# Optimization experiments

Hardware: AMD Instinct MI355X
Metric: run time of the kernel (lower is better)

The kernel has to match this reference:

```python
import jax, jax.numpy as jnp
import numpy as np

H, KV, D, HID = 8, 4, 256, 2560  # heads, kv heads, head_dim, hidden_size
S, L = 32, 8192                  # new seq_len, cache_len
EPS = 1e-6


def setup_inputs() -> dict:
    key = jax.random.key(0)
    ks = jax.random.split(key, 10)
    return {
        "hidden_states": jax.random.normal(ks[0], (S, HID), jnp.float32),
        "cos": jax.random.uniform(ks[1], (S, D), jnp.float32, -1.0, 1.0),
        "sin": jax.random.uniform(ks[2], (S, D), jnp.float32, -1.0, 1.0),
        "cache_k": jax.random.normal(ks[3], (KV, L, D), jnp.float32),
        "cache_v": jax.random.normal(ks[4], (KV, L, D), jnp.float32),
        "mask": jnp.zeros((1, S, L), jnp.float32),
        "W_q": jax.random.normal(ks[5], (HID, H * D), jnp.float32) * 0.02,
        "W_k": jax.random.normal(ks[6], (HID, KV * D), jnp.float32) * 0.02,
        "W_v": jax.random.normal(ks[7], (HID, KV * D), jnp.float32) * 0.02,
        "W_o": jax.random.normal(ks[8], (H * D, HID), jnp.float32) * 0.02,
        "q_norm_w": jnp.ones((D,), jnp.float32),
        "k_norm_w": jnp.ones((D,), jnp.float32),
        "v_norm_w": jnp.ones((D,), jnp.float32),
    }


def _rms(x, w):
    return x * jax.lax.rsqrt(jnp.mean(x * x, axis=-1, keepdims=True) + EPS) * w


def _rope(x, cos, sin):
    # x: [h, S, D]; cos/sin: [S, D] broadcast over head axis
    half = x.shape[-1] // 2
    rot = jnp.concatenate([-x[..., half:], x[..., :half]], axis=-1)
    return x * cos + rot * sin


def reference(hidden_states, cos, sin, cache_k, cache_v, mask,
              W_q, W_k, W_v, W_o, q_norm_w, k_norm_w, v_norm_w):
    G = H // KV  # kv groups
    s = hidden_states.shape[0]
    l = cache_k.shape[1]

    q = (hidden_states @ W_q).reshape(s, H, D).transpose(1, 0, 2)   # [H,S,D]
    q = _rope(_rms(q, q_norm_w), cos, sin)
    k = (hidden_states @ W_k).reshape(s, KV, D).transpose(1, 0, 2)  # [KV,S,D]
    k = _rope(_rms(k, k_norm_w), cos, sin)
    v = _rms((hidden_states @ W_v).reshape(s, KV, D).transpose(1, 0, 2), v_norm_w)

    # sliding-window KV cache roll: drop oldest s, append new
    ck = jnp.concatenate([cache_k[:, s:, :], k], axis=1)  # [KV,L,D]
    cv = jnp.concatenate([cache_v[:, s:, :], v], axis=1)  # [KV,L,D]

    qg = q.reshape(KV, G * s, D)
    attn = jnp.einsum('knd,kld->knl', qg, ck).reshape(H, s, l)  # no 1/sqrt(D), per source
    attn = jax.nn.softmax(attn + mask, axis=-1).reshape(KV, G * s, l)
    out = jnp.einsum('knl,kld->knd', attn, cv)                   # [KV,G*S,D]
    out = out.reshape(H, s, D).transpose(1, 0, 2).reshape(s, H * D)
    return out @ W_o
```

## Files before the change

kernel.cpp:

```cpp
#include <hip/hip_runtime.h>
#include <hip/hip_bf16.h>
#include <cstdint>
#include <cstddef>

#define H_     8
#define KV_    4
#define D_     256
#define HID_   2560
#define S_     32
#define L_     8192
#define NQ_    64
#define LKEEP_ (L_ - S_)

__global__ __launch_bounds__(256) void k_qkv(
    const float* __restrict__ hidden,
    const float* __restrict__ Wq, const float* __restrict__ Wk, const float* __restrict__ Wv,
    float* __restrict__ part)
{
    const int col0  = blockIdx.x * 512;
    const int kbase = blockIdx.y * 80;
    const float* W; int ldw, wb;
    if (col0 < 2048)      { W = Wq; ldw = 2048; wb = col0; }
    else if (col0 < 3072) { W = Wk; ldw = 1024; wb = col0 - 2048; }
    else                  { W = Wv; ldw = 1024; wb = col0 - 3072; }
    const int tid = threadIdx.x;
    const int tc  = tid * 2;

    __shared__ __align__(16) float hsT[80][36];
    for (int i = 0; i < 3; i++) {
        int idx = i * 256 + tid;
        if (idx < 640) {
            int r = idx / 20, c4 = idx % 20;
            float4 v = *(const float4*)&hidden[r * HID_ + kbase + c4 * 4];
            hsT[c4*4+0][r] = v.x; hsT[c4*4+1][r] = v.y;
            hsT[c4*4+2][r] = v.z; hsT[c4*4+3][r] = v.w;
        }
    }
    __syncthreads();

    const float* Wt = W + (size_t)kbase * ldw + wb + tc;
    float acc[32][2] = {};
#define LW(k) (*(const float2*)&Wt[(size_t)(k) * ldw])
#define FMABLK(k, wc) \
    _Pragma("unroll") for (int r4 = 0; r4 < 8; r4++) { \
      float4 h = *(const float4*)&hsT[(k)][r4*4]; \
      acc[r4*4+0][0] = fmaf(h.x, wc.x, acc[r4*4+0][0]); acc[r4*4+0][1] = fmaf(h.x, wc.y, acc[r4*4+0][1]); \
      acc[r4*4+1][0] = fmaf(h.y, wc.x, acc[r4*4+1][0]); acc[r4*4+1][1] = fmaf(h.y, wc.y, acc[r4*4+1][1]); \
      acc[r4*4+2][0] = fmaf(h.z, wc.x, acc[r4*4+2][0]); acc[r4*4+2][1] = fmaf(h.z, wc.y, acc[r4*4+2][1]); \
      acc[r4*4+3][0] = fmaf(h.w, wc.x, acc[r4*4+3][0]); acc[r4*4+3][1] = fmaf(h.w, wc.y, acc[r4*4+3][1]); }
#define STEPL(wreg, k) { float2 wc = wreg; wreg = LW((k) + 8); FMABLK(k, wc) }
#define STEPN(wreg, k) { float2 wc = wreg; FMABLK(k, wc) }

    float2 w0=LW(0),w1=LW(1),w2=LW(2),w3=LW(3),w4=LW(4),w5=LW(5),w6=LW(6),w7=LW(7);
    for (int ib = 0; ib <= 64; ib += 8) {
        STEPL(w0, ib+0) STEPL(w1, ib+1) STEPL(w2, ib+2) STEPL(w3, ib+3)
        STEPL(w4, ib+4) STEPL(w5, ib+5) STEPL(w6, ib+6) STEPL(w7, ib+7)
    }
    STEPN(w0, 72) STEPN(w1, 73) STEPN(w2, 74) STEPN(w3, 75)
    STEPN(w4, 76) STEPN(w5, 77) STEPN(w6, 78) STEPN(w7, 79)
#undef STEPL
#undef STEPN
#undef FMABLK
#undef LW
    float* op = part + (size_t)blockIdx.y * (32 * 4096);
    #pragma unroll
    for (int r = 0; r < 32; r++)
        *(float2*)&op[r * 4096 + col0 + tc] = make_float2(acc[r][0], acc[r][1]);
}

__global__ __launch_bounds__(256) void k_rms_rope(
    const float* __restrict__ part,
    const float* __restrict__ cosb, const float* __restrict__ sinb,
    const float* __restrict__ qw, const float* __restrict__ kw, const float* __restrict__ vw,
    float* __restrict__ q, float* __restrict__ kn, float* __restrict__ vn)
{
    const int b = blockIdx.x;
    const int th = b >> 5;
    const int s  = b & 31;
    const int d  = threadIdx.x;
    const float* w; float* op; int col; bool rope;
    if (th < 8)       { w = qw; col = th * 256;               op = q  + ((size_t)(th * 32 + s)) * 256;        rope = true;  }
    else if (th < 12) { w = kw; col = 2048 + (th - 8) * 256;  op = kn + ((size_t)((th - 8) * 32 + s)) * 256;  rope = true;  }
    else              { w = vw; col = 3072 + (th - 12) * 256; op = vn + ((size_t)((th - 12) * 32 + s)) * 256; rope = false; }
    const int base = s * 4096 + col + d;
    float a0 = 0.f, a1 = 0.f, a2 = 0.f, a3 = 0.f;
    #pragma unroll
    for (int p = 0; p < 32; p += 4) {
        a0 += part[(size_t)(p + 0) * 131072 + base];
        a1 += part[(size_t)(p + 1) * 131072 + base];
        a2 += part[(size_t)(p + 2) * 131072 + base];
        a3 += part[(size_t)(p + 3) * 131072 + base];
    }
    float x = (a0 + a1) + (a2 + a3);
    float ss = x * x;
    #pragma unroll
    for (int m = 32; m; m >>= 1) ss += __shfl_xor(ss, m, 64);
    __shared__ float red[4];
    __shared__ float xs[256];
    if ((threadIdx.x & 63) == 0) red[threadIdx.x >> 6] = ss;
    __syncthreads();
    float tot = red[0] + red[1] + red[2] + red[3];
    float xn = x * rsqrtf(tot * (1.0f / 256.0f) + 1e-6f) * w[d];
    xs[d] = xn;
    __syncthreads();
    float out = xn;
    if (rope) {
        float rot = (d < 128) ? -xs[d + 128] : xs[d - 128];
        out = xn * cosb[s * 256 + d] + rot * sinb[s * 256 + d];
    }
    op[d] = out;
}

__global__ __launch_bounds__(512) void k_qk(
    const float* __restrict__ qb,
    const float* __restrict__ cache_k,
    const float* __restrict__ knb,
    const float* __restrict__ mask,
    float* __restrict__ logits)
{
    const int l0 = blockIdx.x * 128;
    const int kh = blockIdx.y;
    const int tid = threadIdx.x;
    const int r0 = (tid >> 6) * 8;
    const int c0 = (tid & 63) * 2;

    __shared__ __align__(16) float ks[2][32][132];
    __shared__ __align__(16) float qsq[2][64][36];

    float acc[8][2] = {};

    {
        int qq = tid >> 3, dq = tid & 7;
        *(float4*)&qsq[0][qq][dq * 4] =
            *(const float4*)&qb[((size_t)kh * 64 + qq) * 256 + dq * 4];
        #pragma unroll
        for (int i = 0; i < 2; i++) {
            int idx = i * 512 + tid;
            int l = idx >> 3, d4 = idx & 7;
            int labs = l0 + l;
            const float* src = (labs < LKEEP_)
                ? (cache_k + ((size_t)kh * L_ + labs + S_) * 256 + d4 * 4)
                : (knb + ((size_t)kh * S_ + (labs - LKEEP_)) * 256 + d4 * 4);
            float4 v = *(const float4*)src;
            ks[0][d4 * 4 + 0][l] = v.x; ks[0][d4 * 4 + 1][l] = v.y;
            ks[0][d4 * 4 + 2][l] = v.z; ks[0][d4 * 4 + 3][l] = v.w;
        }
    }
    __syncthreads();

    for (int dc = 0; dc < 8; dc++) {
        const int cur = dc & 1, nxt = cur ^ 1;
        if (dc < 7) {
            const int d0 = (dc + 1) * 32;
            {
                int qq = tid >> 3, dq = tid & 7;
                *(float4*)&qsq[nxt][qq][dq * 4] =
                    *(const float4*)&qb[((size_t)kh * 64 + qq) * 256 + d0 + dq * 4];
            }
            #pragma unroll
            for (int i = 0; i < 2; i++) {
                int idx = i * 512 + tid;
                int l = idx >> 3, d4 = idx & 7;
                int labs = l0 + l;
                const float* src = (labs < LKEEP_)
                    ? (cache_k + ((size_t)kh * L_ + labs + S_) * 256 + d0 + d4 * 4)
                    : (knb + ((size_t)kh * S_ + (labs - LKEEP_)) * 256 + d0 + d4 * 4);
                float4 v = *(const float4*)src;
                ks[nxt][d4 * 4 + 0][l] = v.x; ks[nxt][d4 * 4 + 1][l] = v.y;
                ks[nxt][d4 * 4 + 2][l] = v.z; ks[nxt][d4 * 4 + 3][l] = v.w;
            }
        }
        #pragma unroll
        for (int d4 = 0; d4 < 8; d4++) {
            float4 qv[8];
            #pragma unroll
            for (int i = 0; i < 8; i++)
                qv[i] = *(const float4*)&qsq[cur][r0 + i][d4 * 4];
            float2 k0 = *(const float2*)&ks[cur][d4 * 4 + 0][c0];
            float2 k1 = *(const float2*)&ks[cur][d4 * 4 + 1][c0];
            float2 k2 = *(const float2*)&ks[cur][d4 * 4 + 2][c0];
            float2 k3 = *(const float2*)&ks[cur][d4 * 4 + 3][c0];
            #pragma unroll
            for (int i = 0; i < 8; i++) {
                acc[i][0] = fmaf(qv[i].x, k0.x, acc[i][0]); acc[i][1] = fmaf(qv[i].x, k0.y, acc[i][1]);
                acc[i][0] = fmaf(qv[i].y, k1.x, acc[i][0]); acc[i][1] = fmaf(qv[i].y, k1.y, acc[i][1]);
                acc[i][0] = fmaf(qv[i].z, k2.x, acc[i][0]); acc[i][1] = fmaf(qv[i].z, k2.y, acc[i][1]);
                acc[i][0] = fmaf(qv[i].w, k3.x, acc[i][0]); acc[i][1] = fmaf(qv[i].w, k3.y, acc[i][1]);
            }
        }
        __syncthreads();
    }
    #pragma unroll
    for (int i = 0; i < 8; i++) {
        int qq = r0 + i, s = qq & 31;
        float2 m2 = *(const float2*)&mask[(size_t)s * L_ + l0 + c0];
        *(float2*)&logits[((size_t)kh * NQ_ + qq) * L_ + l0 + c0] =
            make_float2(acc[i][0] + m2.x, acc[i][1] + m2.y);
    }
}

__global__ __launch_bounds__(256) void k_rowstat(
    const float* __restrict__ logits,
    float* __restrict__ rowmax, float* __restrict__ rowsum)
{
    const int r = blockIdx.x;
    const int tid = threadIdx.x;
    const float* lp = logits + (size_t)r * L_;
    float m = -1e30f, s = 0.f;
    for (int i = tid; i < L_; i += 256) {
        float x = lp[i];
        float nm = fmaxf(m, x);
        s = s * __expf(m - nm) + __expf(x - nm);
        m = nm;
    }
    #pragma unroll
    for (int off = 32; off; off >>= 1) {
        float m2 = __shfl_xor(m, off, 64);
        float s2 = __shfl_xor(s, off, 64);
        float nm = fmaxf(m, m2);
        s = s * __expf(m - nm) + s2 * __expf(m2 - nm);
        m = nm;
    }
    __shared__ float rm[4], rs[4];
    if ((tid & 63) == 0) { rm[tid >> 6] = m; rs[tid >> 6] = s; }
    __syncthreads();
    if (tid == 0) {
        float M = fmaxf(fmaxf(rm[0], rm[1]), fmaxf(rm[2], rm[3]));
        float S = rs[0] * __expf(rm[0] - M) + rs[1] * __expf(rm[1] - M)
                + rs[2] * __expf(rm[2] - M) + rs[3] * __expf(rm[3] - M);
        rowmax[r] = M;
        rowsum[r] = S;
    }
}

__global__ __launch_bounds__(512) void k_pv(
    const float* __restrict__ logits,
    const float* __restrict__ rowmax,
    const float* __restrict__ cache_v, const float* __restrict__ vnb,
    float* __restrict__ pvpart)
{
    const int l0 = blockIdx.x * 128;
    const int kh = blockIdx.y;
    const int tid = threadIdx.x;
    const int r0 = (tid >> 6) * 8;
    const int c0 = (tid & 63) * 4;

    __shared__ __align__(16) float ps[64][132];
    __shared__ __align__(16) float vs[2][16][260];

    #pragma unroll
    for (int i = 0; i < 4; i++) {
        int idx = i * 512 + tid;
        int qq = idx >> 5, lq = idx & 31;
        float4 v = *(const float4*)&logits[((size_t)kh * NQ_ + qq) * L_ + l0 + lq * 4];
        float rm = rowmax[kh * NQ_ + qq];
        v.x = __expf(v.x - rm); v.y = __expf(v.y - rm);
        v.z = __expf(v.z - rm); v.w = __expf(v.w - rm);
        *(float4*)&ps[qq][lq * 4] = v;
    }
    #pragma unroll
    for (int i = 0; i < 2; i++) {
        int idx = i * 512 + tid;
        int l = idx >> 6, dq = idx & 63;
        int labs = l0 + l;
        const float* src = (labs < LKEEP_)
            ? (cache_v + ((size_t)kh * L_ + labs + S_) * 256 + dq * 4)
            : (vnb + ((size_t)kh * S_ + (labs - LKEEP_)) * 256 + dq * 4);
        *(float4*)&vs[0][l][dq * 4] = *(const float4*)src;
    }
    __syncthreads();

    float acc[8][4] = {};
    for (int lc = 0; lc < 8; lc++) {
        const int cur = lc & 1, nxt = cur ^ 1;
        if (lc < 7) {
            #pragma unroll
            for (int i = 0; i < 2; i++) {
                int idx = i * 512 + tid;
                int l = idx >> 6, dq = idx & 63;
                int labs = l0 + (lc + 1) * 16 + l;
                const float* src = (labs < LKEEP_)
                    ? (cache_v + ((size_t)kh * L_ + labs + S_) * 256 + dq * 4)
                    : (vnb + ((size_t)kh * S_ + (labs - LKEEP_)) * 256 + dq * 4);
                *(float4*)&vs[nxt][l][dq * 4] = *(const float4*)src;
            }
        }
        #pragma unroll
        for (int lg = 0; lg < 4; lg++) {
            float4 pv[8];
            #pragma unroll
            for (int i = 0; i < 8; i++)
                pv[i] = *(const float4*)&ps[r0 + i][lc * 16 + lg * 4];
            float4 v0 = *(const float4*)&vs[cur][lg * 4 + 0][c0];
            float4 v1 = *(const float4*)&vs[cur][lg * 4 + 1][c0];
            float4 v2 = *(const float4*)&vs[cur][lg * 4 + 2][c0];
            float4 v3 = *(const float4*)&vs[cur][lg * 4 + 3][c0];
            #pragma unroll
            for (int i = 0; i < 8; i++) {
                acc[i][0] = fmaf(pv[i].x, v0.x, acc[i][0]); acc[i][1] = fmaf(pv[i].x, v0.y, acc[i][1]);
                acc[i][2] = fmaf(pv[i].x, v0.z, acc[i][2]); acc[i][3] = fmaf(pv[i].x, v0.w, acc[i][3]);
                acc[i][0] = fmaf(pv[i].y, v1.x, acc[i][0]); acc[i][1] = fmaf(pv[i].y, v1.y, acc[i][1]);
                acc[i][2] = fmaf(pv[i].y, v1.z, acc[i][2]); acc[i][3] = fmaf(pv[i].y, v1.w, acc[i][3]);
                acc[i][0] = fmaf(pv[i].z, v2.x, acc[i][0]); acc[i][1] = fmaf(pv[i].z, v2.y, acc[i][1]);
                acc[i][2] = fmaf(pv[i].z, v2.z, acc[i][2]); acc[i][3] = fmaf(pv[i].z, v2.w, acc[i][3]);
                acc[i][0] = fmaf(pv[i].w, v3.x, acc[i][0]); acc[i][1] = fmaf(pv[i].w, v3.y, acc[i][1]);
                acc[i][2] = fmaf(pv[i].w, v3.z, acc[i][2]); acc[i][3] = fmaf(pv[i].w, v3.w, acc[i][3]);
            }
        }
        __syncthreads();
    }
    float* op = pvpart + (((size_t)kh * 64 + blockIdx.x) * NQ_) * 256;
    #pragma unroll
    for (int i = 0; i < 8; i++)
        *(float4*)&op[(r0 + i) * 256 + c0] =
            make_float4(acc[i][0], acc[i][1], acc[i][2], acc[i][3]);
}

__global__ __launch_bounds__(256) void k_pvcomb(
    const float* __restrict__ pvpart, const float* __restrict__ rowsum,
    float* __restrict__ attn)
{
    const int b = blockIdx.x;
    const int kh = b >> 6, n = b & 63;
    const int d = threadIdx.x;
    const float* pp = pvpart + ((size_t)kh * 64 * NQ_ + n) * 256 + d;
    float s0 = 0.f, s1 = 0.f, s2 = 0.f, s3 = 0.f;
    for (int c = 0; c < 64; c += 4) {
        s0 += pp[(size_t)(c + 0) * (NQ_ * 256)];
        s1 += pp[(size_t)(c + 1) * (NQ_ * 256)];
        s2 += pp[(size_t)(c + 2) * (NQ_ * 256)];
        s3 += pp[(size_t)(c + 3) * (NQ_ * 256)];
    }
    float sum = (s0 + s1) + (s2 + s3);
    const int h = kh * 2 + (n >> 5), s = n & 31;
    attn[(size_t)s * 2048 + h * 256 + d] = sum / rowsum[b];
}

__global__ __launch_bounds__(256) void k_out(
    const float* __restrict__ attn, const float* __restrict__ Wo,
    float* __restrict__ opart)
{
    const int col0  = blockIdx.x * 512;
    const int kbase = blockIdx.y * 64;
    const int tid   = threadIdx.x;
    const int tc    = tid * 2;

    __shared__ __align__(16) float hsT[64][36];
    #pragma unroll
    for (int i = 0; i < 2; i++) {
        int idx = i * 256 + tid;
        int r = idx >> 4, c4 = idx & 15;
        float4 v = *(const float4*)&attn[r * 2048 + kbase + c4 * 4];
        hsT[c4*4+0][r] = v.x; hsT[c4*4+1][r] = v.y;
        hsT[c4*4+2][r] = v.z; hsT[c4*4+3][r] = v.w;
    }
    __syncthreads();

    const float* Wt = Wo + (size_t)kbase * 2560 + col0 + tc;
    float acc[32][2] = {};
#define LW(k) (*(const float2*)&Wt[(size_t)(k) * 2560])
#define FMABLK(k, wc) \
    _Pragma("unroll") for (int r4 = 0; r4 < 8; r4++) { \
      float4 h = *(const float4*)&hsT[(k)][r4*4]; \
      acc[r4*4+0][0] = fmaf(h.x, wc.x, acc[r4*4+0][0]); acc[r4*4+0][1] = fmaf(h.x, wc.y, acc[r4*4+0][1]); \
      acc[r4*4+1][0] = fmaf(h.y, wc.x, acc[r4*4+1][0]); acc[r4*4+1][1] = fmaf(h.y, wc.y, acc[r4*4+1][1]); \
      acc[r4*4+2][0] = fmaf(h.z, wc.x, acc[r4*4+2][0]); acc[r4*4+2][1] = fmaf(h.z, wc.y, acc[r4*4+2][1]); \
      acc[r4*4+3][0] = fmaf(h.w, wc.x, acc[r4*4+3][0]); acc[r4*4+3][1] = fmaf(h.w, wc.y, acc[r4*4+3][1]); }
#define STEPL(wreg, k) { float2 wc = wreg; wreg = LW((k) + 8); FMABLK(k, wc) }
#define STEPN(wreg, k) { float2 wc = wreg; FMABLK(k, wc) }

    float2 w0=LW(0),w1=LW(1),w2=LW(2),w3=LW(3),w4=LW(4),w5=LW(5),w6=LW(6),w7=LW(7);
    for (int ib = 0; ib <= 48; ib += 8) {
        STEPL(w0, ib+0) STEPL(w1, ib+1) STEPL(w2, ib+2) STEPL(w3, ib+3)
        STEPL(w4, ib+4) STEPL(w5, ib+5) STEPL(w6, ib+6) STEPL(w7, ib+7)
    }
    STEPN(w0, 56) STEPN(w1, 57) STEPN(w2, 58) STEPN(w3, 59)
    STEPN(w4, 60) STEPN(w5, 61) STEPN(w6, 62) STEPN(w7, 63)
#undef STEPL
#undef STEPN
#undef FMABLK
#undef LW
    float* op = opart + (size_t)blockIdx.y * (32 * 2560);
    #pragma unroll
    for (int r = 0; r < 32; r++)
        *(float2*)&op[r * 2560 + col0 + tc] = make_float2(acc[r][0], acc[r][1]);
}

__global__ __launch_bounds__(256) void k_osum(const float* __restrict__ opart,
                                              float* __restrict__ out)
{
    int idx = blockIdx.x * 256 + threadIdx.x;
    float a0 = 0.f, a1 = 0.f, a2 = 0.f, a3 = 0.f;
    #pragma unroll
    for (int p = 0; p < 32; p += 4) {
        a0 += opart[(size_t)(p + 0) * 81920 + idx];
        a1 += opart[(size_t)(p + 1) * 81920 + idx];
        a2 += opart[(size_t)(p + 2) * 81920 + idx];
        a3 += opart[(size_t)(p + 3) * 81920 + idx];
    }
    out[idx] = (a0 + a1) + (a2 + a3);
}

extern "C" void kernel_launch(void* const* d_in, const int* in_sizes, int n_in,
                              void* d_out, int out_size, void* d_ws, size_t ws_size,
                              hipStream_t stream)
{
    const float* hidden  = (const float*)d_in[0];
    const float* cosb    = (const float*)d_in[1];
    const float* sinb    = (const float*)d_in[2];
    const float* cache_k = (const float*)d_in[3];
    const float* cache_v = (const float*)d_in[4];
    const float* mask    = (const float*)d_in[5];
    const float* Wq      = (const float*)d_in[6];
    const float* Wk      = (const float*)d_in[7];
    const float* Wv      = (const float*)d_in[8];
    const float* Wo      = (const float*)d_in[9];
    const float* qw      = (const float*)d_in[10];
    const float* kw      = (const float*)d_in[11];
    const float* vw      = (const float*)d_in[12];

    float* ws = (float*)d_ws;
    float* A      = ws;
    float* logits = ws + 4194304;
    float* qb     = ws + 6291456;
    float* knb    = ws + 6356992;
    float* vnb    = ws + 6389760;
    float* rowmax = ws + 6422528;
    float* rowsum = ws + 6422784;
    float* attn   = ws + 6423040;

    float* qkvp   = A;
    float* pvpart = A;
    float* opart  = A;

    k_qkv<<<dim3(8, 32), 256, 0, stream>>>(hidden, Wq, Wk, Wv, qkvp);
    k_rms_rope<<<512, 256, 0, stream>>>(qkvp, cosb, sinb, qw, kw, vw, qb, knb, vnb);
    k_qk<<<dim3(64, 4), 512, 0, stream>>>(qb, cache_k, knb, mask, logits);
    k_rowstat<<<256, 256, 0, stream>>>(logits, rowmax, rowsum);
    k_pv<<<dim3(64, 4), 512, 0, stream>>>(logits, rowmax, cache_v, vnb, pvpart);
    k_pvcomb<<<256, 256, 0, stream>>>(pvpart, rowsum, attn);
    k_out<<<dim3(5, 32), 256, 0, stream>>>(attn, Wo, opart);
    k_osum<<<320, 256, 0, stream>>>(opart, (float*)d_out);
}
```

Baseline: 246.4 us.

## Fuse QK, softmax and PV into split-K flash-decoding attention kernel

Replaces the separate QK-logits, row-statistics and PV kernels with one kernel. Each block handles a 64-position chunk of the cache for one KV head, computes local max and sum, and writes unnormalised partial outputs. The combine kernel then rescales the 128 chunk partials by their local max and sum. This avoids writing and re-reading the full logits buffer and drops two launches, at the cost of a larger partial-output buffer and more combine work. The projection GEMMs also get a deeper 16-row weight prefetch and 8-way partial-sum accumulation.

```diff
diff --git a/kernel.cpp b/kernel.cpp
--- a/kernel.cpp
+++ b/kernel.cpp
@@ -11,6 +11,7 @@
 #define L_     8192
 #define NQ_    64
 #define LKEEP_ (L_ - S_)
+#define NCH_   128
 
 __global__ __launch_bounds__(256) void k_qkv(
     const float* __restrict__ hidden,
@@ -40,7 +41,6 @@
 
     const float* Wt = W + (size_t)kbase * ldw + wb + tc;
     float acc[32][2] = {};
-#define LW(k) (*(const float2*)&Wt[(size_t)(k) * ldw])
 #define FMABLK(k, wc) \
     _Pragma("unroll") for (int r4 = 0; r4 < 8; r4++) { \
       float4 h = *(const float4*)&hsT[(k)][r4*4]; \
@@ -48,20 +48,22 @@
       acc[r4*4+1][0] = fmaf(h.y, wc.x, acc[r4*4+1][0]); acc[r4*4+1][1] = fmaf(h.y, wc.y, acc[r4*4+1][1]); \
       acc[r4*4+2][0] = fmaf(h.z, wc.x, acc[r4*4+2][0]); acc[r4*4+2][1] = fmaf(h.z, wc.y, acc[r4*4+2][1]); \
       acc[r4*4+3][0] = fmaf(h.w, wc.x, acc[r4*4+3][0]); acc[r4*4+3][1] = fmaf(h.w, wc.y, acc[r4*4+3][1]); }
-#define STEPL(wreg, k) { float2 wc = wreg; wreg = LW((k) + 8); FMABLK(k, wc) }
-#define STEPN(wreg, k) { float2 wc = wreg; FMABLK(k, wc) }
-
-    float2 w0=LW(0),w1=LW(1),w2=LW(2),w3=LW(3),w4=LW(4),w5=LW(5),w6=LW(6),w7=LW(7);
-    for (int ib = 0; ib <= 64; ib += 8) {
-        STEPL(w0, ib+0) STEPL(w1, ib+1) STEPL(w2, ib+2) STEPL(w3, ib+3)
-        STEPL(w4, ib+4) STEPL(w5, ib+5) STEPL(w6, ib+6) STEPL(w7, ib+7)
-    }
-    STEPN(w0, 72) STEPN(w1, 73) STEPN(w2, 74) STEPN(w3, 75)
-    STEPN(w4, 76) STEPN(w5, 77) STEPN(w6, 78) STEPN(w7, 79)
-#undef STEPL
-#undef STEPN
+
+    float2 wr[16];
+    #pragma unroll
+    for (int j = 0; j < 16; j++) wr[j] = *(const float2*)&Wt[(size_t)j * ldw];
+    for (int ib = 0; ib < 64; ib += 16) {
+        #pragma unroll
+        for (int j = 0; j < 16; j++) {
+            float2 wc = wr[j];
+            wr[j] = *(const float2*)&Wt[(size_t)(ib + j + 16) * ldw];
+            FMABLK(ib + j, wc)
+        }
+    }
+    #pragma unroll
+    for (int j = 0; j < 16; j++) { float2 wc = wr[j]; FMABLK(64 + j, wc) }
 #undef FMABLK
-#undef LW
+
     float* op = part + (size_t)blockIdx.y * (32 * 4096);
     #pragma unroll
     for (int r = 0; r < 32; r++)
@@ -83,15 +85,14 @@
     else if (th < 12) { w = kw; col = 2048 + (th - 8) * 256;  op = kn + ((size_t)((th - 8) * 32 + s)) * 256;  rope = true;  }
     else              { w = vw; col = 3072 + (th - 12) * 256; op = vn + ((size_t)((th - 12) * 32 + s)) * 256; rope = false; }
     const int base = s * 4096 + col + d;
-    float a0 = 0.f, a1 = 0.f, a2 = 0.f, a3 = 0.f;
-    #pragma unroll
-    for (int p = 0; p < 32; p += 4) {
-        a0 += part[(size_t)(p + 0) * 131072 + base];
-        a1 += part[(size_t)(p + 1) * 131072 + base];
-        a2 += part[(size_t)(p + 2) * 131072 + base];
-        a3 += part[(size_t)(p + 3) * 131072 + base];
-    }
-    float x = (a0 + a1) + (a2 + a3);
+    float a[8] = {};
+    #pragma unroll
+    for (int p = 0; p < 32; p += 8) {
+        #pragma unroll
+        for (int j = 0; j < 8; j++)
+            a[j] += part[(size_t)(p + j) * 131072 + base];
+    }
+    float x = ((a[0]+a[1])+(a[2]+a[3])) + ((a[4]+a[5])+(a[6]+a[7]));
     float ss = x * x;
     #pragma unroll
     for (int m = 32; m; m >>= 1) ss += __shfl_xor(ss, m, 64);
@@ -111,229 +112,190 @@
     op[d] = out;
 }
 
-__global__ __launch_bounds__(512) void k_qk(
+__global__ __launch_bounds__(512) void k_attn(
     const float* __restrict__ qb,
-    const float* __restrict__ cache_k,
-    const float* __restrict__ knb,
+    const float* __restrict__ cache_k, const float* __restrict__ knb,
+    const float* __restrict__ cache_v, const float* __restrict__ vnb,
     const float* __restrict__ mask,
-    float* __restrict__ logits)
-{
-    const int l0 = blockIdx.x * 128;
-    const int kh = blockIdx.y;
-    const int tid = threadIdx.x;
-    const int r0 = (tid >> 6) * 8;
-    const int c0 = (tid & 63) * 2;
-
-    __shared__ __align__(16) float ks[2][32][132];
-    __shared__ __align__(16) float qsq[2][64][36];
-
-    float acc[8][2] = {};
-
-    {
-        int qq = tid >> 3, dq = tid & 7;
-        *(float4*)&qsq[0][qq][dq * 4] =
-            *(const float4*)&qb[((size_t)kh * 64 + qq) * 256 + dq * 4];
+    float* __restrict__ pvpart,
+    float* __restrict__ mstat,
+    float* __restrict__ lstat)
+{
+    const int chunk = blockIdx.x;
+    const int kh    = blockIdx.y;
+    const int l0    = chunk * 64;
+    const int tid   = threadIdx.x;
+    const int lane  = tid & 63;
+    const int r0    = (tid >> 6) * 8;
+
+    __shared__ __align__(16) float qs[64][68];
+    __shared__ __align__(16) float ks[64][64];
+    __shared__ __align__(16) float ps[64][68];
+    __shared__ __align__(16) float vs[2][8][260];
+
+    float s[8] = {};
+    for (int dch = 0; dch < 4; dch++) {
+        const int d0 = dch * 64;
         #pragma unroll
         for (int i = 0; i < 2; i++) {
             int idx = i * 512 + tid;
-            int l = idx >> 3, d4 = idx & 7;
+            int qq = idx >> 4, g = idx & 15;
+            *(float4*)&qs[qq][g * 4] =
+                *(const float4*)&qb[((size_t)kh * 64 + qq) * 256 + d0 + g * 4];
+        }
+        #pragma unroll
+        for (int i = 0; i < 2; i++) {
+            int idx = i * 512 + tid;
+            int l = idx >> 4, g = idx & 15;
             int labs = l0 + l;
             const float* src = (labs < LKEEP_)
-                ? (cache_k + ((size_t)kh * L_ + labs + S_) * 256 + d4 * 4)
-                : (knb + ((size_t)kh * S_ + (labs - LKEEP_)) * 256 + d4 * 4);
-            float4 v = *(const float4*)src;
-            ks[0][d4 * 4 + 0][l] = v.x; ks[0][d4 * 4 + 1][l] = v.y;
-            ks[0][d4 * 4 + 2][l] = v.z; ks[0][d4 * 4 + 3][l] = v.w;
-        }
-    }
-    __syncthreads();
-
-    for (int dc = 0; dc < 8; dc++) {
-        const int cur = dc & 1, nxt = cur ^ 1;
-        if (dc < 7) {
-            const int d0 = (dc + 1) * 32;
-            {
-                int qq = tid >> 3, dq = tid & 7;
-                *(float4*)&qsq[nxt][qq][dq * 4] =
-                    *(const float4*)&qb[((size_t)kh * 64 + qq) * 256 + d0 + dq * 4];
-            }
-            #pragma unroll
-            for (int i = 0; i < 2; i++) {
-                int idx = i * 512 + tid;
-                int l = idx >> 3, d4 = idx & 7;
-                int labs = l0 + l;
-                const float* src = (labs < LKEEP_)
-                    ? (cache_k + ((size_t)kh * L_ + labs + S_) * 256 + d0 + d4 * 4)
-                    : (knb + ((size_t)kh * S_ + (labs - LKEEP_)) * 256 + d0 + d4 * 4);
-                float4 v = *(const float4*)src;
-                ks[nxt][d4 * 4 + 0][l] = v.x; ks[nxt][d4 * 4 + 1][l] = v.y;
-                ks[nxt][d4 * 4 + 2][l] = v.z; ks[nxt][d4 * 4 + 3][l] = v.w;
-            }
-        }
-        #pragma unroll
-        for (int d4 = 0; d4 < 8; d4++) {
-            float4 qv[8];
-            #pragma unroll
-            for (int i = 0; i < 8; i++)
-                qv[i] = *(const float4*)&qsq[cur][r0 + i][d4 * 4];
-            float2 k0 = *(const float2*)&ks[cur][d4 * 4 + 0][c0];
-            float2 k1 = *(const float2*)&ks[cur][d4 * 4 + 1][c0];
-            float2 k2 = *(const float2*)&ks[cur][d4 * 4 + 2][c0];
-            float2 k3 = *(const float2*)&ks[cur][d4 * 4 + 3][c0];
+                ? &cache_k[((size_t)kh * L_ + labs + S_) * 256 + d0 + g * 4]
+                : &knb[((size_t)kh * S_ + (labs - LKEEP_)) * 256 + d0 + g * 4];
+            *(float4*)&ks[l][(g ^ (l & 15)) * 4] = *(const float4*)src;
+        }
+        __syncthreads();
+        #pragma unroll
+        for (int g = 0; g < 16; g++) {
+            float4 kv = *(const float4*)&ks[lane][(g ^ (lane & 15)) * 4];
             #pragma unroll
             for (int i = 0; i < 8; i++) {
-                acc[i][0] = fmaf(qv[i].x, k0.x, acc[i][0]); acc[i][1] = fmaf(qv[i].x, k0.y, acc[i][1]);
-                acc[i][0] = fmaf(qv[i].y, k1.x, acc[i][0]); acc[i][1] = fmaf(qv[i].y, k1.y, acc[i][1]);
-                acc[i][0] = fmaf(qv[i].z, k2.x, acc[i][0]); acc[i][1] = fmaf(qv[i].z, k2.y, acc[i][1]);
-                acc[i][0] = fmaf(qv[i].w, k3.x, acc[i][0]); acc[i][1] = fmaf(qv[i].w, k3.y, acc[i][1]);
+                float4 qv = *(const float4*)&qs[r0 + i][g * 4];
+                s[i] = fmaf(qv.x, kv.x, s[i]);
+                s[i] = fmaf(qv.y, kv.y, s[i]);
+                s[i] = fmaf(qv.z, kv.z, s[i]);
+                s[i] = fmaf(qv.w, kv.w, s[i]);
             }
         }
         __syncthreads();
     }
+
+    #pragma unroll
+    for (int i = 0; i < 8; i++)
+        s[i] += mask[(size_t)((r0 + i) & 31) * L_ + l0 + lane];
+    float mloc[8], lloc[8];
     #pragma unroll
     for (int i = 0; i < 8; i++) {
-        int qq = r0 + i, s = qq & 31;
-        float2 m2 = *(const float2*)&mask[(size_t)s * L_ + l0 + c0];
-        *(float2*)&logits[((size_t)kh * NQ_ + qq) * L_ + l0 + c0] =
-            make_float2(acc[i][0] + m2.x, acc[i][1] + m2.y);
-    }
-}
-
-__global__ __launch_bounds__(256) void k_rowstat(
-    const float* __restrict__ logits,
-    float* __restrict__ rowmax, float* __restrict__ rowsum)
-{
-    const int r = blockIdx.x;
-    const int tid = threadIdx.x;
-    const float* lp = logits + (size_t)r * L_;
-    float m = -1e30f, s = 0.f;
-    for (int i = tid; i < L_; i += 256) {
-        float x = lp[i];
-        float nm = fmaxf(m, x);
-        s = s * __expf(m - nm) + __expf(x - nm);
-        m = nm;
-    }
-    #pragma unroll
-    for (int off = 32; off; off >>= 1) {
-        float m2 = __shfl_xor(m, off, 64);
-        float s2 = __shfl_xor(s, off, 64);
-        float nm = fmaxf(m, m2);
-        s = s * __expf(m - nm) + s2 * __expf(m2 - nm);
-        m = nm;
-    }
-    __shared__ float rm[4], rs[4];
-    if ((tid & 63) == 0) { rm[tid >> 6] = m; rs[tid >> 6] = s; }
-    __syncthreads();
-    if (tid == 0) {
-        float M = fmaxf(fmaxf(rm[0], rm[1]), fmaxf(rm[2], rm[3]));
-        float S = rs[0] * __expf(rm[0] - M) + rs[1] * __expf(rm[1] - M)
-                + rs[2] * __expf(rm[2] - M) + rs[3] * __expf(rm[3] - M);
-        rowmax[r] = M;
-        rowsum[r] = S;
-    }
-}
-
-__global__ __launch_bounds__(512) void k_pv(
-    const float* __restrict__ logits,
-    const float* __restrict__ rowmax,
-    const float* __restrict__ cache_v, const float* __restrict__ vnb,
-    float* __restrict__ pvpart)
-{
-    const int l0 = blockIdx.x * 128;
-    const int kh = blockIdx.y;
-    const int tid = threadIdx.x;
-    const int r0 = (tid >> 6) * 8;
-    const int c0 = (tid & 63) * 4;
-
-    __shared__ __align__(16) float ps[64][132];
-    __shared__ __align__(16) float vs[2][16][260];
-
-    #pragma unroll
-    for (int i = 0; i < 4; i++) {
-        int idx = i * 512 + tid;
-        int qq = idx >> 5, lq = idx & 31;
-        float4 v = *(const float4*)&logits[((size_t)kh * NQ_ + qq) * L_ + l0 + lq * 4];
-        float rm = rowmax[kh * NQ_ + qq];
-        v.x = __expf(v.x - rm); v.y = __expf(v.y - rm);
-        v.z = __expf(v.z - rm); v.w = __expf(v.w - rm);
-        *(float4*)&ps[qq][lq * 4] = v;
-    }
-    #pragma unroll
-    for (int i = 0; i < 2; i++) {
-        int idx = i * 512 + tid;
-        int l = idx >> 6, dq = idx & 63;
+        float mm = s[i];
+        #pragma unroll
+        for (int off = 32; off; off >>= 1) mm = fmaxf(mm, __shfl_xor(mm, off, 64));
+        float pp = __expf(s[i] - mm);
+        float ssum = pp;
+        #pragma unroll
+        for (int off = 32; off; off >>= 1) ssum += __shfl_xor(ssum, off, 64);
+        mloc[i] = mm; lloc[i] = ssum;
+        ps[r0 + i][lane] = pp;
+    }
+    if (lane == 0) {
+        #pragma unroll
+        for (int i = 0; i < 8; i++) {
+            mstat[((size_t)chunk * KV_ + kh) * 64 + r0 + i] = mloc[i];
+            lstat[((size_t)chunk * KV_ + kh) * 64 + r0 + i] = lloc[i];
+        }
+    }
+
+    {
+        int l = tid >> 6, dg = tid & 63;
         int labs = l0 + l;
         const float* src = (labs < LKEEP_)
-            ? (cache_v + ((size_t)kh * L_ + labs + S_) * 256 + dq * 4)
-            : (vnb + ((size_t)kh * S_ + (labs - LKEEP_)) * 256 + dq * 4);
-        *(float4*)&vs[0][l][dq * 4] = *(const float4*)src;
-    }
-    __syncthreads();
-
-    float acc[8][4] = {};
-    for (int lc = 0; lc < 8; lc++) {
-        const int cur = lc & 1, nxt = cur ^ 1;
-        if (lc < 7) {
-            #pragma unroll
-            for (int i = 0; i < 2; i++) {
-                int idx = i * 512 + tid;
-                int l = idx >> 6, dq = idx & 63;
-                int labs = l0 + (lc + 1) * 16 + l;
-                const float* src = (labs < LKEEP_)
-                    ? (cache_v + ((size_t)kh * L_ + labs + S_) * 256 + dq * 4)
-                    : (vnb + ((size_t)kh * S_ + (labs - LKEEP_)) * 256 + dq * 4);
-                *(float4*)&vs[nxt][l][dq * 4] = *(const float4*)src;
-            }
-        }
-        #pragma unroll
-        for (int lg = 0; lg < 4; lg++) {
+            ? &cache_v[((size_t)kh * L_ + labs + S_) * 256 + dg * 4]
+            : &vnb[((size_t)kh * S_ + (labs - LKEEP_)) * 256 + dg * 4];
+        *(float4*)&vs[0][l][dg * 4] = *(const float4*)src;
+    }
+    __syncthreads();
+    float o[8][4] = {};
+    for (int vc = 0; vc < 8; vc++) {
+        const int cur = vc & 1;
+        if (vc < 7) {
+            int l = tid >> 6, dg = tid & 63;
+            int labs = l0 + (vc + 1) * 8 + l;
+            const float* src = (labs < LKEEP_)
+                ? &cache_v[((size_t)kh * L_ + labs + S_) * 256 + dg * 4]
+                : &vnb[((size_t)kh * S_ + (labs - LKEEP_)) * 256 + dg * 4];
+            *(float4*)&vs[cur ^ 1][l][dg * 4] = *(const float4*)src;
+        }
+        #pragma unroll
+        for (int l4 = 0; l4 < 2; l4++) {
             float4 pv[8];
             #pragma unroll
             for (int i = 0; i < 8; i++)
-                pv[i] = *(const float4*)&ps[r0 + i][lc * 16 + lg * 4];
-            float4 v0 = *(const float4*)&vs[cur][lg * 4 + 0][c0];
-            float4 v1 = *(const float4*)&vs[cur][lg * 4 + 1][c0];
-            float4 v2 = *(const float4*)&vs[cur][lg * 4 + 2][c0];
-            float4 v3 = *(const float4*)&vs[cur][lg * 4 + 3][c0];
+                pv[i] = *(const float4*)&ps[r0 + i][vc * 8 + l4 * 4];
             #pragma unroll
-            for (int i = 0; i < 8; i++) {
-                acc[i][0] = fmaf(pv[i].x, v0.x, acc[i][0]); acc[i][1] = fmaf(pv[i].x, v0.y, acc[i][1]);
-                acc[i][2] = fmaf(pv[i].x, v0.z, acc[i][2]); acc[i][3] = fmaf(pv[i].x, v0.w, acc[i][3]);
-                acc[i][0] = fmaf(pv[i].y, v1.x, acc[i][0]); acc[i][1] = fmaf(pv[i].y, v1.y, acc[i][1]);
-                acc[i][2] = fmaf(pv[i].y, v1.z, acc[i][2]); acc[i][3] = fmaf(pv[i].y, v1.w, acc[i][3]);
-                acc[i][0] = fmaf(pv[i].z, v2.x, acc[i][0]); acc[i][1] = fmaf(pv[i].z, v2.y, acc[i][1]);
-                acc[i][2] = fmaf(pv[i].z, v2.z, acc[i][2]); acc[i][3] = fmaf(pv[i].z, v2.w, acc[i][3]);
-                acc[i][0] = fmaf(pv[i].w, v3.x, acc[i][0]); acc[i][1] = fmaf(pv[i].w, v3.y, acc[i][1]);
-                acc[i][2] = fmaf(pv[i].w, v3.z, acc[i][2]); acc[i][3] = fmaf(pv[i].w, v3.w, acc[i][3]);
+            for (int ll = 0; ll < 4; ll++) {
+                float4 vv = *(const float4*)&vs[cur][l4 * 4 + ll][lane * 4];
+                #pragma unroll
+                for (int i = 0; i < 8; i++) {
+                    float pp = ((const float*)&pv[i])[ll];
+                    o[i][0] = fmaf(pp, vv.x, o[i][0]);
+                    o[i][1] = fmaf(pp, vv.y, o[i][1]);
+                    o[i][2] = fmaf(pp, vv.z, o[i][2]);
+                    o[i][3] = fmaf(pp, vv.w, o[i][3]);
+                }
             }
         }
         __syncthreads();
     }
-    float* op = pvpart + (((size_t)kh * 64 + blockIdx.x) * NQ_) * 256;
+    float* op = pvpart + ((size_t)chunk * KV_ + kh) * (64 * 256);
     #pragma unroll
     for (int i = 0; i < 8; i++)
-        *(float4*)&op[(r0 + i) * 256 + c0] =
-            make_float4(acc[i][0], acc[i][1], acc[i][2], acc[i][3]);
+        *(float4*)&op[(r0 + i) * 256 + lane * 4] =
+            make_float4(o[i][0], o[i][1], o[i][2], o[i][3]);
 }
 
 __global__ __launch_bounds__(256) void k_pvcomb(
-    const float* __restrict__ pvpart, const float* __restrict__ rowsum,
+    const float* __restrict__ pvpart,
+    const float* __restrict__ mstat, const float* __restrict__ lstat,
     float* __restrict__ attn)
 {
     const int b = blockIdx.x;
     const int kh = b >> 6, n = b & 63;
-    const int d = threadIdx.x;
-    const float* pp = pvpart + ((size_t)kh * 64 * NQ_ + n) * 256 + d;
-    float s0 = 0.f, s1 = 0.f, s2 = 0.f, s3 = 0.f;
-    for (int c = 0; c < 64; c += 4) {
-        s0 += pp[(size_t)(c + 0) * (NQ_ * 256)];
-        s1 += pp[(size_t)(c + 1) * (NQ_ * 256)];
-        s2 += pp[(size_t)(c + 2) * (NQ_ * 256)];
-        s3 += pp[(size_t)(c + 3) * (NQ_ * 256)];
-    }
-    float sum = (s0 + s1) + (s2 + s3);
-    const int h = kh * 2 + (n >> 5), s = n & 31;
-    attn[(size_t)s * 2048 + h * 256 + d] = sum / rowsum[b];
+    const int tid = threadIdx.x;
+    const int tg = tid >> 6, dl = tid & 63;
+    __shared__ float ms_[NCH_], ls_[NCH_], ws_[NCH_];
+    __shared__ __align__(16) float red[4][64][4];
+
+    if (tid < NCH_) {
+        ms_[tid] = mstat[((size_t)tid * KV_ + kh) * 64 + n];
+        ls_[tid] = lstat[((size_t)tid * KV_ + kh) * 64 + n];
+    }
+    __syncthreads();
+    float M = -1e30f;
+    for (int c = 0; c < NCH_; c++) M = fmaxf(M, ms_[c]);
+    if (tid < NCH_) ws_[tid] = __expf(ms_[tid] - M);
+    __syncthreads();
+    float denom = 0.f;
+    for (int c = 0; c < NCH_; c++) denom += ws_[c] * ls_[c];
+
+    float4 a[8];
+    #pragma unroll
+    for (int j = 0; j < 8; j++) a[j] = make_float4(0.f, 0.f, 0.f, 0.f);
+    for (int cc = 0; cc < 32; cc += 8) {
+        #pragma unroll
+        for (int j = 0; j < 8; j++) {
+            int c = (cc + j) * 4 + tg;
+            float w = ws_[c];
+            float4 v = *(const float4*)&pvpart[(((size_t)c * KV_ + kh) * 64 + n) * 256 + dl * 4];
+            a[j].x = fmaf(w, v.x, a[j].x); a[j].y = fmaf(w, v.y, a[j].y);
+            a[j].z = fmaf(w, v.z, a[j].z); a[j].w = fmaf(w, v.w, a[j].w);
+        }
+    }
+    float4 t;
+    t.x = ((a[0].x+a[1].x)+(a[2].x+a[3].x)) + ((a[4].x+a[5].x)+(a[6].x+a[7].x));
+    t.y = ((a[0].y+a[1].y)+(a[2].y+a[3].y)) + ((a[4].y+a[5].y)+(a[6].y+a[7].y));
+    t.z = ((a[0].z+a[1].z)+(a[2].z+a[3].z)) + ((a[4].z+a[5].z)+(a[6].z+a[7].z));
+    t.w = ((a[0].w+a[1].w)+(a[2].w+a[3].w)) + ((a[4].w+a[5].w)+(a[6].w+a[7].w));
+    *(float4*)&red[tg][dl][0] = t;
+    __syncthreads();
+    if (tid < 64) {
+        float4 r0 = *(const float4*)&red[0][tid][0];
+        float4 r1 = *(const float4*)&red[1][tid][0];
+        float4 r2 = *(const float4*)&red[2][tid][0];
+        float4 r3 = *(const float4*)&red[3][tid][0];
+        float inv = 1.0f / denom;
+        float4 o = make_float4((r0.x+r1.x+r2.x+r3.x) * inv, (r0.y+r1.y+r2.y+r3.y) * inv,
+                               (r0.z+r1.z+r2.z+r3.z) * inv, (r0.w+r1.w+r2.w+r3.w) * inv);
+        const int h = kh * 2 + (n >> 5), srow = n & 31;
+        *(float4*)&attn[(size_t)srow * 2048 + h * 256 + tid * 4] = o;
+    }
 }
 
 __global__ __launch_bounds__(256) void k_out(
@@ -358,7 +320,6 @@
 
     const float* Wt = Wo + (size_t)kbase * 2560 + col0 + tc;
     float acc[32][2] = {};
-#define LW(k) (*(const float2*)&Wt[(size_t)(k) * 2560])
 #define FMABLK(k, wc) \
     _Pragma("unroll") for (int r4 = 0; r4 < 8; r4++) { \
       float4 h = *(const float4*)&hsT[(k)][r4*4]; \
@@ -366,20 +327,22 @@
       acc[r4*4+1][0] = fmaf(h.y, wc.x, acc[r4*4+1][0]); acc[r4*4+1][1] = fmaf(h.y, wc.y, acc[r4*4+1][1]); \
       acc[r4*4+2][0] = fmaf(h.z, wc.x, acc[r4*4+2][0]); acc[r4*4+2][1] = fmaf(h.z, wc.y, acc[r4*4+2][1]); \
       acc[r4*4+3][0] = fmaf(h.w, wc.x, acc[r4*4+3][0]); acc[r4*4+3][1] = fmaf(h.w, wc.y, acc[r4*4+3][1]); }
-#define STEPL(wreg, k) { float2 wc = wreg; wreg = LW((k) + 8); FMABLK(k, wc) }
-#define STEPN(wreg, k) { float2 wc = wreg; FMABLK(k, wc) }
-
-    float2 w0=LW(0),w1=LW(1),w2=LW(2),w3=LW(3),w4=LW(4),w5=LW(5),w6=LW(6),w7=LW(7);
-    for (int ib = 0; ib <= 48; ib += 8) {
-        STEPL(w0, ib+0) STEPL(w1, ib+1) STEPL(w2, ib+2) STEPL(w3, ib+3)
-        STEPL(w4, ib+4) STEPL(w5, ib+5) STEPL(w6, ib+6) STEPL(w7, ib+7)
-    }
-    STEPN(w0, 56) STEPN(w1, 57) STEPN(w2, 58) STEPN(w3, 59)
-    STEPN(w4, 60) STEPN(w5, 61) STEPN(w6, 62) STEPN(w7, 63)
-#undef STEPL
-#undef STEPN
+
+    float2 wr[16];
+    #pragma unroll
+    for (int j = 0; j < 16; j++) wr[j] = *(const float2*)&Wt[(size_t)j * 2560];
+    for (int ib = 0; ib < 48; ib += 16) {
+        #pragma unroll
+        for (int j = 0; j < 16; j++) {
+            float2 wc = wr[j];
+            wr[j] = *(const float2*)&Wt[(size_t)(ib + j + 16) * 2560];
+            FMABLK(ib + j, wc)
+        }
+    }
+    #pragma unroll
+    for (int j = 0; j < 16; j++) { float2 wc = wr[j]; FMABLK(48 + j, wc) }
 #undef FMABLK
-#undef LW
+
     float* op = opart + (size_t)blockIdx.y * (32 * 2560);
     #pragma unroll
     for (int r = 0; r < 32; r++)
@@ -390,15 +353,14 @@
                                               float* __restrict__ out)
 {
     int idx = blockIdx.x * 256 + threadIdx.x;
-    float a0 = 0.f, a1 = 0.f, a2 = 0.f, a3 = 0.f;
-    #pragma unroll
-    for (int p = 0; p < 32; p += 4) {
-        a0 += opart[(size_t)(p + 0) * 81920 + idx];
-        a1 += opart[(size_t)(p + 1) * 81920 + idx];
-        a2 += opart[(size_t)(p + 2) * 81920 + idx];
-        a3 += opart[(size_t)(p + 3) * 81920 + idx];
-    }
-    out[idx] = (a0 + a1) + (a2 + a3);
+    float a[8] = {};
+    #pragma unroll
+    for (int p = 0; p < 32; p += 8) {
+        #pragma unroll
+        for (int j = 0; j < 8; j++)
+            a[j] += opart[(size_t)(p + j) * 81920 + idx];
+    }
+    out[idx] = ((a[0]+a[1])+(a[2]+a[3])) + ((a[4]+a[5])+(a[6]+a[7]));
 }
 
 extern "C" void kernel_launch(void* const* d_in, const int* in_sizes, int n_in,
@@ -421,13 +383,12 @@
 
     float* ws = (float*)d_ws;
     float* A      = ws;
-    float* logits = ws + 4194304;
-    float* qb     = ws + 6291456;
-    float* knb    = ws + 6356992;
-    float* vnb    = ws + 6389760;
-    float* rowmax = ws + 6422528;
-    float* rowsum = ws + 6422784;
-    float* attn   = ws + 6423040;
+    float* qb     = ws + 8388608;
+    float* knb    = ws + 8454144;
+    float* vnb    = ws + 8486912;
+    float* mstat  = ws + 8519680;
+    float* lstat  = ws + 8552448;
+    float* attn   = ws + 8585216;
 
     float* qkvp   = A;
     float* pvpart = A;
@@ -435,10 +396,9 @@
 
     k_qkv<<<dim3(8, 32), 256, 0, stream>>>(hidden, Wq, Wk, Wv, qkvp);
     k_rms_rope<<<512, 256, 0, stream>>>(qkvp, cosb, sinb, qw, kw, vw, qb, knb, vnb);
-    k_qk<<<dim3(64, 4), 512, 0, stream>>>(qb, cache_k, knb, mask, logits);
-    k_rowstat<<<256, 256, 0, stream>>>(logits, rowmax, rowsum);
-    k_pv<<<dim3(64, 4), 512, 0, stream>>>(logits, rowmax, cache_v, vnb, pvpart);
-    k_pvcomb<<<256, 256, 0, stream>>>(pvpart, rowsum, attn);
+    k_attn<<<dim3(NCH_, KV_), 512, 0, stream>>>(qb, cache_k, knb, cache_v, vnb, mask,
+                                                pvpart, mstat, lstat);
+    k_pvcomb<<<256, 256, 0, stream>>>(pvpart, mstat, lstat, attn);
     k_out<<<dim3(5, 32), 256, 0, stream>>>(attn, Wo, opart);
     k_osum<<<320, 256, 0, stream>>>(opart, (float*)d_out);
 }
```

Result: slower. 268.7 us (+9.1%).
